# Kernel tuning notes

Measured on AMD Instinct MI355X. Metric: run time of the kernel, lower is better.

## Reference

```python
import jax, jax.numpy as jnp
import numpy as np

NUM_QUBITS = 16
N_LAYERS = 3
N_PARAMS = 6
BATCH = 64
DIM = 2 ** NUM_QUBITS


def setup_inputs() -> dict:
    key = jax.random.key(0)
    k1, k2, k3, k4, k5 = jax.random.split(key, 5)
    sr = jax.random.normal(k1, (BATCH, DIM), jnp.float32)
    si = jax.random.normal(k2, (BATCH, DIM), jnp.float32)
    nrm = jnp.sqrt(jnp.sum(sr * sr + si * si, axis=1, keepdims=True))
    sr, si = sr / nrm, si / nrm  # StatePrep requires normalized states
    var_params = jax.random.normal(k3, (N_LAYERS, NUM_QUBITS, N_PARAMS), jnp.float32)
    head_w = jax.random.normal(k4, (1, NUM_QUBITS), jnp.float32) / np.sqrt(NUM_QUBITS)
    head_b = jax.random.normal(k5, (1,), jnp.float32) * 0.01
    return {"state_real": sr, "state_imag": si, "var_params": var_params,
            "head_w": head_w, "head_b": head_b}


def _rot_unitary(tx, ty, tz):
    # Fused single-qubit unitary U = RZ(tz) @ RY(ty) @ RX(tx)
    cx, sx = jnp.cos(tx / 2), jnp.sin(tx / 2)
    cy, sy = jnp.cos(ty / 2), jnp.sin(ty / 2)
    Rx = jnp.stack([jnp.stack([cx + 0j, -1j * sx]),
                    jnp.stack([-1j * sx, cx + 0j])])
    Ry = jnp.stack([jnp.stack([cy + 0j, -sy + 0j]),
                    jnp.stack([sy + 0j, cy + 0j])])
    ez = jnp.exp(-1j * tz / 2)
    zero = jnp.zeros_like(ez)
    Rz = jnp.stack([jnp.stack([ez, zero]), jnp.stack([zero, jnp.conj(ez)])])
    return (Rz @ Ry @ Rx).astype(jnp.complex64)


def _circuit_features(state_real, state_imag, var_params):
    psi = jax.lax.complex(state_real, state_imag)  # (B, 2^n), wire 0 = MSB
    B = psi.shape[0]
    for l in range(N_LAYERS):
        for q in range(NUM_QUBITS):
            U = _rot_unitary(var_params[l, q, 0], var_params[l, q, 1], var_params[l, q, 2])
            psi = psi.reshape(B, 2 ** q, 2, -1)  # isolate wire q
            psi = jnp.einsum('ij,bljr->blir', U, psi)
        for q in range(NUM_QUBITS - 1):
            # CNOT(control=q, target=q+1): flip target axis where control=1
            psi = psi.reshape(B, 2 ** q, 2, 2, -1)
            psi = jnp.concatenate([psi[:, :, 0:1], psi[:, :, 1:2, ::-1]], axis=2)
        psi = psi.reshape(B, -1)
    probs = psi.real ** 2 + psi.imag ** 2  # (B, 2^n)
    feats = []
    for q in range(NUM_QUBITS):
        p = probs.reshape(B, 2 ** q, 2, -1)
        feats.append(p[:, :, 0, :].sum(axis=(1, 2)) - p[:, :, 1, :].sum(axis=(1, 2)))
    return jnp.stack(feats, axis=1)  # (B, n) expvals of PauliZ


def reference(state_real, state_imag, var_params, head_w, head_b):
    feats = _circuit_features(state_real, state_imag, var_params)
    return (feats @ head_w.T + head_b)[:, 0]  # (B,)
```

## Files before the change

kernel.cpp:

```cpp
#include <hip/hip_runtime.h>


typedef float f2 __attribute__((ext_vector_type(2)));

struct G8 { float r00,i00,r01,i01,r10,i10,r11,i11; };

__device__ __forceinline__ f2 mkf2(float a, float b) { f2 r; r.x = a; r.y = b; return r; }
__device__ __forceinline__ f2 swp(f2 v) { f2 r; r.x = v.y; r.y = v.x; return r; }
__device__ __forceinline__ f2 sn(f2 v) { f2 r; r.x = -v.y; r.y = v.x; return r; }
__device__ __forceinline__ f2 shf2(f2 v, int mask) {
  return mkf2(__shfl_xor(v.x, mask), __shfl_xor(v.y, mask));
}

__device__ __forceinline__ G8 loadG(const float* p) {
  G8 g;
  g.r00=p[0]; g.i00=p[1]; g.r01=p[2]; g.i01=p[3];
  g.r10=p[4]; g.i10=p[5]; g.r11=p[6]; g.i11=p[7];
  return g;
}

struct CP { f2 dr, di, br, bi; };
__device__ __forceinline__ CP mkCP(const G8& g, int w) {
  CP c;
  const float a = w ? g.r11 : g.r00, b = w ? g.i11 : g.i00;
  const float p = w ? g.r10 : g.r01, q = w ? g.i10 : g.i01;
  c.dr = mkf2(a,a); c.di = mkf2(b,b); c.br = mkf2(p,p); c.bi = mkf2(q,q);
  return c;
}
__device__ __forceinline__ void supdP(const CP& c, f2& x, f2 p) {
  x = __builtin_elementwise_fma(c.dr, x,
       __builtin_elementwise_fma(c.di, sn(x),
        __builtin_elementwise_fma(c.br, p, c.bi * sn(p))));
}

struct C2 { f2 dr, di, br, bi; };
__device__ __forceinline__ C2 mkC2(const G8& g, int wlo, int whi) {
  C2 c;
  c.dr = mkf2(wlo ? g.r11 : g.r00, whi ? g.r11 : g.r00);
  c.di = mkf2(wlo ? g.i11 : g.i00, whi ? g.i11 : g.i00);
  c.br = mkf2(wlo ? g.r10 : g.r01, whi ? g.r10 : g.r01);
  c.bi = mkf2(wlo ? g.i10 : g.i01, whi ? g.i10 : g.i01);
  return c;
}
__device__ __forceinline__ void supd2(const C2& c, f2& xr, f2& xi, f2 pr, f2 pi) {
  f2 nr = __builtin_elementwise_fma(c.dr, xr,
           __builtin_elementwise_fma(c.di, -xi,
            __builtin_elementwise_fma(c.br, pr, c.bi * (-pi))));
  f2 ni = __builtin_elementwise_fma(c.dr, xi,
           __builtin_elementwise_fma(c.di, xr,
            __builtin_elementwise_fma(c.br, pi, c.bi * pr)));
  xr = nr; xi = ni;
}

__device__ __forceinline__ void buildU(const float* __restrict__ vp, float* U) {
  const int i = threadIdx.x;
  if (i < 48) {
    const float tx = vp[i*6+0], ty = vp[i*6+1], tz = vp[i*6+2];
    float sx, cx, sy, cy, sz, cz;
    sincosf(0.5f*tx, &sx, &cx);
    sincosf(0.5f*ty, &sy, &cy);
    sincosf(0.5f*tz, &sz, &cz);
    const float m00r = cy*cx,  m00i = sy*sx;
    const float m01r = -sy*cx, m01i = -cy*sx;
    const float m10r = sy*cx,  m10i = -cy*sx;
    const float m11r = cy*cx,  m11i = -sy*sx;
    float* o = U + i*8;
    o[0] = cz*m00r + sz*m00i;  o[1] = cz*m00i - sz*m00r;
    o[2] = cz*m01r + sz*m01i;  o[3] = cz*m01i - sz*m01r;
    o[4] = cz*m10r - sz*m10i;  o[5] = cz*m10i + sz*m10r;
    o[6] = cz*m11r - sz*m11i;  o[7] = cz*m11i + sz*m11r;
  }
}

#define GU(l, w) loadG(Ush + ((l)*16 + (w))*8)

__global__ void __launch_bounds__(256, 2)
kA(const float* __restrict__ sr, const float* __restrict__ si,
   float* __restrict__ dr, float* __restrict__ di,
   const float* __restrict__ vp, const float* __restrict__ hb, float* __restrict__ out) {
  __shared__ float Ush[384];
  buildU(vp, Ush);
  const int t = threadIdx.x;
  const int l = t & 63, wv = t >> 6;
  const int l5 = (l >> 5) & 1, l4 = (l >> 4) & 1;
  const int b = blockIdx.x >> 3, c = blockIdx.x & 7;
  if (blockIdx.x == 0 && t < 64) out[t] = hb[0];
  __syncthreads();

  const size_t bb = (size_t)b << 16;
  const int tb = (l5 << 10) | (l4 << 9) | (c << 6) | (wv << 4) | (l & 15);
  f2 x[32];
  #pragma unroll
  for (int k = 0; k < 32; ++k) {
    const size_t a = bb + (k << 11) + tb;
    x[k] = mkf2(sr[a], si[a]);
  }

#define RPA(CA, CB, A, B) { f2 tt = x[A]; supdP(CA, x[A], x[B]); supdP(CB, x[B], tt); }

  #pragma unroll
  for (int g = 0; g < 5; ++g) {
    const int kb = 4 - g;
    const G8 U = GU(0, g);
    const CP c0 = mkCP(U, 0), c1 = mkCP(U, 1);
    #pragma unroll
    for (int p = 0; p < 16; ++p) {
      const int i0 = ((p >> kb) << (kb + 1)) | (p & ((1 << kb) - 1));
      RPA(c0, c1, i0, i0 | (1 << kb));
    }
  }
  { const G8 U = GU(0,5); const CP cc = mkCP(U, l5);
    #pragma unroll
    for (int a = 0; a < 32; ++a) supdP(cc, x[a], shf2(x[a], 32)); }
  { const G8 U = GU(0,6); const CP cc = mkCP(U, l4);
    #pragma unroll
    for (int a = 0; a < 32; ++a) supdP(cc, x[a], shf2(x[a], 16)); }
  { const G8 U = GU(1,0); const CP c0 = mkCP(U,0), c1 = mkCP(U,1);
    #pragma unroll
    for (int k = 0; k < 32; ++k) if (!((k>>4)&1)) RPA(c0, c1, k, k^24); }
  { const G8 U = GU(1,1); const CP c0 = mkCP(U,0), c1 = mkCP(U,1);
    #pragma unroll
    for (int k = 0; k < 32; ++k) if (!((k>>3)&1)) {
      const int f = (k>>4)&1;
      RPA(f?c1:c0, f?c0:c1, k, k^12);
    } }
  { const G8 U = GU(1,2); const CP c0 = mkCP(U,0), c1 = mkCP(U,1);
    #pragma unroll
    for (int k = 0; k < 32; ++k) if (!((k>>2)&1)) {
      const int f = ((k>>4)^(k>>3))&1;
      RPA(f?c1:c0, f?c0:c1, k, k^6);
    } }
  { const G8 U = GU(1,3); const CP c0 = mkCP(U,0), c1 = mkCP(U,1);
    #pragma unroll
    for (int k = 0; k < 32; ++k) if (!((k>>1)&1)) {
      const int f = ((k>>4)^(k>>3)^(k>>2))&1;
      RPA(f?c1:c0, f?c0:c1, k, k^3);
    } }
  { const G8 U = GU(1,4); const CP c0 = mkCP(U,0), c1 = mkCP(U,1);
    #pragma unroll
    for (int m = 0; m < 16; ++m) {
      const int k0 = 2*m, k1 = 2*m+1;
      f2 p0 = shf2(x[k1], 32), p1 = shf2(x[k0], 32);
      const int w0 = __builtin_popcount(k0)&1;
      supdP(w0?c1:c0, x[k0], p0);
      supdP(w0?c0:c1, x[k1], p1);
    } }
  { const G8 U = GU(2,0); const CP c0 = mkCP(U,0), c1 = mkCP(U,1);
    #pragma unroll
    for (int k = 0; k < 32; ++k) if (!((k>>4)&1)) RPA(c0, c1, k, k^20); }
  { const G8 U = GU(2,1); const CP c0 = mkCP(U,0), c1 = mkCP(U,1);
    #pragma unroll
    for (int k = 0; k < 32; ++k) if (!((k>>3)&1)) RPA(c0, c1, k, k^10); }
  { const G8 U = GU(2,2); const CP c0 = mkCP(U,0), c1 = mkCP(U,1);
    #pragma unroll
    for (int k = 0; k < 32; ++k) if (!((k>>2)&1)) {
      const int f = (k>>4)&1;
      RPA(f?c1:c0, f?c0:c1, k, k^5);
    } }

  #pragma unroll
  for (int k = 0; k < 32; ++k) {
    const size_t a = bb + (k << 11) + tb;
    dr[a] = x[k].x; di[a] = x[k].y;
  }
#undef RPA
}

__device__ __forceinline__ int SA2(int i) { return i ^ (((i >> 5) & 7) << 1); }

__global__ void __launch_bounds__(256, 2)
kB(const float* __restrict__ sr, const float* __restrict__ si,
   const float* __restrict__ vp, const float* __restrict__ hw, float* __restrict__ out) {
  __shared__ float lds[16384];
  __shared__ float Ush[384];
  __shared__ float red[4];
  buildU(vp, Ush);
  const int t = threadIdx.x;
  const int l = t & 63, wv = t >> 6;
  const int b = blockIdx.x >> 3, h3 = blockIdx.x & 7;
  __syncthreads();

  const int P   = __builtin_popcount(h3) & 1;
  const int h14 = (h3 >> 1) & 1;
  const int pA  = (h3 ^ (h3 >> 2)) & 1;
  const size_t base0 = ((size_t)b << 16) | (h3 << 13) | (wv << 8) | (l << 2);

  f2 xr2[16], xi2[16];
  #pragma unroll
  for (int kk = 0; kk < 4; ++kk) {
    const float4 r0 = *(const float4*)(sr + base0 + (kk << 10));
    const float4 r1 = *(const float4*)(sr + base0 + (kk << 10) + 4096);
    const float4 i0 = *(const float4*)(si + base0 + (kk << 10));
    const float4 i1 = *(const float4*)(si + base0 + (kk << 10) + 4096);
    xr2[kk*4+0] = mkf2(r0.x, r1.x); xr2[kk*4+1] = mkf2(r0.y, r1.y);
    xr2[kk*4+2] = mkf2(r0.z, r1.z); xr2[kk*4+3] = mkf2(r0.w, r1.w);
    xi2[kk*4+0] = mkf2(i0.x, i1.x); xi2[kk*4+1] = mkf2(i0.y, i1.y);
    xi2[kk*4+2] = mkf2(i0.z, i1.z); xi2[kk*4+3] = mkf2(i0.w, i1.w);
  }

#define RP2(CA, CB, A, B) { f2 tr = xr2[A], ti = xi2[A]; \
    supd2(CA, xr2[A], xi2[A], xr2[B], xi2[B]); \
    supd2(CB, xr2[B], xi2[B], tr, ti); }

  #pragma unroll
  for (int g = 0; g < 6; ++g) {
    const int mask = 32 >> g;
    const G8 U = GU(0, 8 + g);
    const int hi = (l >> (5 - g)) & 1;
    const C2 cc = mkC2(U, hi, hi);
    #pragma unroll
    for (int s = 0; s < 16; ++s) {
      f2 pr = shf2(xr2[s], mask), pi = shf2(xi2[s], mask);
      supd2(cc, xr2[s], xi2[s], pr, pi);
    }
  }
  { const G8 U = GU(0,14);
    const C2 c0 = mkC2(U,0,0), c1 = mkC2(U,1,1);
    #pragma unroll
    for (int kk = 0; kk < 4; ++kk)
      #pragma unroll
      for (int e0 = 0; e0 < 2; ++e0) RP2(c0, c1, kk*4+e0, kk*4+e0+2); }
  { const G8 U = GU(0,15);
    const C2 c0 = mkC2(U,0,0), c1 = mkC2(U,1,1);
    #pragma unroll
    for (int kk = 0; kk < 4; ++kk) {
      RP2(c0, c1, kk*4+0, kk*4+1);
      RP2(c0, c1, kk*4+2, kk*4+3);
    } }

  #pragma unroll
  for (int s = 0; s < 16; ++s) {
    const int i0 = (((s >> 2) << 10) | (wv << 8) | (l << 2) | (s & 3)) << 1;
    *(f2*)&lds[SA2(i0)] = xr2[s];
    *(f2*)&lds[8192 + SA2(i0)] = xi2[s];
  }
  __syncthreads();
  #pragma unroll
  for (int m = 0; m < 16; ++m) {
    const int i2 = (((m << 8) | (l << 2) | wv)) << 1;
    xr2[m] = *(f2*)&lds[SA2(i2)];
    xi2[m] = *(f2*)&lds[8192 + SA2(i2)];
  }

  const int l5=(l>>5)&1, l4=(l>>4)&1, l3=(l>>3)&1, l2=(l>>2)&1, l1=(l>>1)&1, l0=l&1;
  { const G8 U = GU(0,7);
    const C2 c0 = mkC2(U,0,0), c1 = mkC2(U,1,1);
    #pragma unroll
    for (int m = 0; m < 16; m += 2) RP2(c0, c1, m, m^1); }
  { const G8 U = GU(1,5);
    const C2 cA = mkC2(U, P, P^1), cB = mkC2(U, P^1, P);
    #pragma unroll
    for (int m = 0; m < 16; ++m) if (!((m>>2)&1)) {
      const int f = (m>>3)&1;
      RP2(f?cB:cA, f?cA:cB, m, m^6);
    } }
  { const G8 U = GU(1,6);
    const C2 cA = mkC2(U, P, P^1), cB = mkC2(U, P^1, P);
    #pragma unroll
    for (int m = 0; m < 16; ++m) if (!((m>>1)&1)) {
      const int f = ((m>>3)^(m>>2))&1;
      RP2(f?cB:cA, f?cA:cB, m, m^3);
    } }
  { const G8 U = GU(1,7);
    const C2 cA = mkC2(U, P, P^1), cB = mkC2(U, P^1, P);
    #pragma unroll
    for (int m = 0; m < 16; m += 2) {
      f2 p0r = shf2(xr2[m^1],32), p0i = shf2(xi2[m^1],32);
      f2 p1r = shf2(xr2[m],32),   p1i = shf2(xi2[m],32);
      const int f = __builtin_popcount(m)&1;
      supd2(f?cB:cA, xr2[m], xi2[m], p0r, p0i);
      supd2(f?cA:cB, xr2[m^1], xi2[m^1], p1r, p1i);
    } }
  #pragma unroll
  for (int g = 0; g < 5; ++g) {
    const int mask = 48 >> g;
    const G8 U = GU(1, 8 + g);
    const int lp = (g==0)? l5 : (g==1)? (l4^l5) : (g==2)? (l3^l4^l5)
                 : (g==3)? (l2^l3^l4^l5) : (l1^l2^l3^l4^l5);
    const C2 cA = mkC2(U, lp^P, lp^P^1), cB = mkC2(U, lp^P^1, lp^P);
    #pragma unroll
    for (int m = 0; m < 16; ++m) {
      f2 pr = shf2(xr2[m], mask), pi = shf2(xi2[m], mask);
      supd2((__builtin_popcount(m)&1)?cB:cA, xr2[m], xi2[m], pr, pi);
    }
  }
  { const G8 U = GU(2,3);
    const C2 cc = mkC2(U, h14, h14^1);
    #pragma unroll
    for (int m = 0; m < 16; ++m) if (!((m>>2)&1)) {
      f2 tr = xr2[m], ti = xi2[m];
      supd2(cc, xr2[m], xi2[m], swp(xr2[m^4]), swp(xi2[m^4]));
      supd2(cc, xr2[m^4], xi2[m^4], swp(tr), swp(ti));
    } }
  { const G8 U = GU(2,4);
    const C2 cA = mkC2(U, pA, pA), cB = mkC2(U, pA^1, pA^1);
    #pragma unroll
    for (int m = 0; m < 16; ++m) if (!((m>>3)&1)) RP2(cA, cB, m, m^10); }
  { const G8 U = GU(2,5);
    const C2 cA = mkC2(U, h14, h14^1), cB = mkC2(U, h14^1, h14);
    #pragma unroll
    for (int m = 0; m < 16; ++m) if (!((m>>2)&1)) RP2(cA, cB, m, m^5); }
  { const G8 U = GU(2,6);
    const C2 cA = mkC2(U, pA, pA), cB = mkC2(U, pA^1, pA^1);
    #pragma unroll
    for (int m = 0; m < 16; ++m) if (!((m>>1)&1)) {
      f2 p0r = shf2(xr2[m^2],32), p0i = shf2(xi2[m^2],32);
      f2 p1r = shf2(xr2[m],32),   p1i = shf2(xi2[m],32);
      const int f = (m>>3)&1;
      supd2(f?cB:cA, xr2[m], xi2[m], p0r, p0i);
      supd2(f?cA:cB, xr2[m^2], xi2[m^2], p1r, p1i);
    } }
  { const G8 U = GU(2,7);
    const C2 cA = mkC2(U, h14, h14^1), cB = mkC2(U, h14^1, h14);
    #pragma unroll
    for (int m = 0; m < 16; m += 2) {
      f2 p0r = shf2(xr2[m^1],16), p0i = shf2(xi2[m^1],16);
      f2 p1r = shf2(xr2[m],16),   p1i = shf2(xi2[m],16);
      const int f = (m>>2)&1;
      supd2(f?cB:cA, xr2[m], xi2[m], p0r, p0i);
      supd2(f?cA:cB, xr2[m^1], xi2[m^1], p1r, p1i);
    } }
  #pragma unroll
  for (int g = 0; g < 3; ++g) {
    const int mask = (g == 0) ? 40 : (g == 1) ? 20 : 10;
    const G8 U = GU(2, 8 + g);
    int lp, mpar, blo, bhi;
    if      (g == 0) { lp = l5;      mpar = 0x0A; blo = lp^pA;  bhi = lp^pA; }
    else if (g == 1) { lp = l4;      mpar = 0x05; blo = lp^h14; bhi = lp^h14^1; }
    else             { lp = l3^l5;   mpar = 0x0A; blo = lp^pA;  bhi = lp^pA; }
    const C2 cA = mkC2(U, blo, bhi), cB = mkC2(U, blo^1, bhi^1);
    #pragma unroll
    for (int m = 0; m < 16; ++m) {
      f2 pr = shf2(xr2[m], mask), pi = shf2(xi2[m], mask);
      supd2((__builtin_popcount(m & mpar)&1)?cB:cA, xr2[m], xi2[m], pr, pi);
    }
  }

  __syncthreads();
  #pragma unroll
  for (int m = 0; m < 16; ++m) {
    const int i2 = (((m << 8) | (l << 2) | wv)) << 1;
    *(f2*)&lds[SA2(i2)] = xr2[m];
    *(f2*)&lds[8192 + SA2(i2)] = xi2[m];
  }
  __syncthreads();
  #pragma unroll
  for (int s = 0; s < 16; ++s) {
    const int i0 = (((s >> 2) << 10) | (wv << 8) | (l << 2) | (s & 3)) << 1;
    xr2[s] = *(f2*)&lds[SA2(i0)];
    xi2[s] = *(f2*)&lds[8192 + SA2(i0)];
  }

  const int wv1 = (wv >> 1) & 1, wv0 = wv & 1;
  const int RPlo = (__builtin_popcount(l) ^ __builtin_popcount(wv) ^ P) & 1;
  const int oddT = (l1 ^ l3 ^ l5 ^ wv1 ^ pA) & 1;
  const int evlo = (l0 ^ l2 ^ l4 ^ wv0 ^ h14) & 1;
  { const G8 U = GU(1,13);
    const C2 cA = mkC2(U, RPlo, RPlo^1), cB = mkC2(U, RPlo^1, RPlo);
    #pragma unroll
    for (int kk = 0; kk < 4; ++kk) {
      const C2& cc = (__builtin_popcount(kk)&1) ? cB : cA;
      #pragma unroll
      for (int e0 = 0; e0 < 2; ++e0) {
        const int a = kk*4 + e0, a2 = a + 2;
        f2 par = shf2(xr2[a2],1), pai = shf2(xi2[a2],1);
        f2 pbr = shf2(xr2[a],1),  pbi = shf2(xi2[a],1);
        supd2(cc, xr2[a],  xi2[a],  par, pai);
        supd2(cc, xr2[a2], xi2[a2], pbr, pbi);
      }
    } }
  { const G8 U = GU(1,14);
    const C2 cA = mkC2(U, RPlo, RPlo^1), cB = mkC2(U, RPlo^1, RPlo);
    #pragma unroll
    for (int kk = 0; kk < 4; ++kk) {
      const int f = __builtin_popcount(kk)&1;
      RP2(f?cB:cA, f?cA:cB, kk*4+0, kk*4+3);
      RP2(f?cB:cA, f?cA:cB, kk*4+1, kk*4+2);
    } }
  { const G8 U = GU(1,15);
    const C2 cA = mkC2(U, RPlo, RPlo^1), cB = mkC2(U, RPlo^1, RPlo);
    #pragma unroll
    for (int kk = 0; kk < 4; ++kk) {
      const int f = __builtin_popcount(kk)&1;
      RP2(f?cB:cA, f?cA:cB, kk*4+0, kk*4+1);
      RP2(f?cA:cB, f?cB:cA, kk*4+2, kk*4+3);
    } }
  { const G8 U = GU(2,11);
    const int b4 = (l2 ^ l4 ^ wv0) & 1;
    const C2 cA = mkC2(U, b4^h14, b4^h14^1), cB = mkC2(U, b4^h14^1, b4^h14);
    #pragma unroll
    for (int s = 0; s < 16; ++s) {
      f2 pr = shf2(xr2[s], 5), pi = shf2(xi2[s], 5);
      supd2(((s>>2)&1)?cB:cA, xr2[s], xi2[s], pr, pi);
    } }
  { const G8 U = GU(2,12);
    const C2 cA = mkC2(U, oddT, oddT), cB = mkC2(U, oddT^1, oddT^1);
    #pragma unroll
    for (int kk = 0; kk < 4; ++kk) {
      const C2& cc = ((kk>>1)&1) ? cB : cA;
      #pragma unroll
      for (int e0 = 0; e0 < 2; ++e0) {
        const int a = kk*4 + e0, a2 = a + 2;
        f2 par = shf2(xr2[a2],2), pai = shf2(xi2[a2],2);
        f2 pbr = shf2(xr2[a],2),  pbi = shf2(xi2[a],2);
        supd2(cc, xr2[a],  xi2[a],  par, pai);
        supd2(cc, xr2[a2], xi2[a2], pbr, pbi);
      }
    } }
  { const G8 U = GU(2,13);
    const C2 cA = mkC2(U, evlo, evlo^1), cB = mkC2(U, evlo^1, evlo);
    #pragma unroll
    for (int kk = 0; kk < 4; ++kk) {
      const C2& cc = (kk&1) ? cB : cA;
      #pragma unroll
      for (int e0 = 0; e0 < 4; e0 += 2) {
        const int a = kk*4 + e0, a2 = a + 1;
        f2 par = shf2(xr2[a2],1), pai = shf2(xi2[a2],1);
        f2 pbr = shf2(xr2[a],1),  pbi = shf2(xi2[a],1);
        supd2(cc, xr2[a],  xi2[a],  par, pai);
        supd2(cc, xr2[a2], xi2[a2], pbr, pbi);
      }
    } }
  { const G8 U = GU(2,14);
    const C2 cA = mkC2(U, oddT, oddT), cB = mkC2(U, oddT^1, oddT^1);
    #pragma unroll
    for (int kk = 0; kk < 4; ++kk) {
      const int f = (kk>>1)&1;
      RP2(f?cB:cA, f?cA:cB, kk*4+0, kk*4+2);
      RP2(f?cB:cA, f?cA:cB, kk*4+1, kk*4+3);
    } }
  { const G8 U = GU(2,15);
    const C2 cA = mkC2(U, evlo, evlo^1), cB = mkC2(U, evlo^1, evlo);
    #pragma unroll
    for (int kk = 0; kk < 4; ++kk) {
      const int f = kk&1;
      RP2(f?cB:cA, f?cA:cB, kk*4+0, kk*4+1);
      RP2(f?cB:cA, f?cA:cB, kk*4+2, kk*4+3);
    } }

  #pragma unroll
  for (int s = 0; s < 16; ++s)
    xr2[s] = xr2[s]*xr2[s] + xi2[s]*xi2[s];
  const int jloc = (h3 << 13) | (wv << 8) | (l << 2);
  float hsum = 0.f;
  #pragma unroll
  for (int q = 0; q < 16; ++q) {
    const int M = (0x3333 << (15 - q)) & 0xFFFF;
    f2 acc = mkf2(0.f, 0.f);
    #pragma unroll
    for (int s = 0; s < 16; ++s) {
      const int amp = ((s >> 2) << 10) | (s & 3);
      if (__builtin_popcount(amp & M) & 1) acc -= xr2[s]; else acc += xr2[s];
    }
    float sv = acc.x + (((M >> 12) & 1) ? -acc.y : acc.y);
    if (__builtin_popcount(jloc & M) & 1) sv = -sv;
    hsum += hw[q] * sv;
  }
  #pragma unroll
  for (int o = 32; o >= 1; o >>= 1) hsum += __shfl_xor(hsum, o);
  if ((t & 63) == 0) red[wv] = hsum;
  __syncthreads();
  if (t == 0) atomicAdd(out + b, red[0] + red[1] + red[2] + red[3]);
#undef RP2
}

extern "C" void kernel_launch(void* const* d_in, const int* in_sizes, int n_in,
                              void* d_out, int out_size, void* d_ws, size_t ws_size,
                              hipStream_t stream) {
  const float* in_r = (const float*)d_in[0];
  const float* in_i = (const float*)d_in[1];
  const float* vp = (const float*)d_in[2];
  const float* hw = (const float*)d_in[3];
  const float* hb = (const float*)d_in[4];
  float* out = (float*)d_out;

  float* ws_r = (float*)d_ws;
  float* ws_i = ws_r + 4194304ull;

  kA<<<512, 256, 0, stream>>>(in_r, in_i, ws_r, ws_i, vp, hb, out);
  kB<<<512, 256, 0, stream>>>(ws_r, ws_i, vp, hw, out);
}
```

Measured before the change: 141.5 us.

## Split kB tiles in half and move two gates into kA

Moves gates (1,5) and (2,3) from the second kernel into the first, so one more wire becomes block-fixed in kB. kB can then give each block a 4096-amplitude slice instead of 8192, launching 1024 blocks with half the registers and LDS per thread and a launch bound of 4 blocks per CU. The intent is higher occupancy and better latency hiding in kB. The cost is more shuffle work in kA, and all the parity and index bookkeeping had to be re-derived, which risks correctness.

```diff
diff --git a/kernel.cpp b/kernel.cpp
--- a/kernel.cpp
+++ b/kernel.cpp
@@ -145,6 +145,12 @@
       supdP(w0?c1:c0, x[k0], p0);
       supdP(w0?c0:c1, x[k1], p1);
     } }
+  { const G8 U = GU(1,5); const CP cA = mkCP(U, l5), cB = mkCP(U, l5^1);
+    #pragma unroll
+    for (int k = 0; k < 32; ++k) {
+      f2 p = shf2(x[k], 48);
+      supdP((__builtin_popcount(k)&1)?cB:cA, x[k], p);
+    } }
   { const G8 U = GU(2,0); const CP c0 = mkCP(U,0), c1 = mkCP(U,1);
     #pragma unroll
     for (int k = 0; k < 32; ++k) if (!((k>>4)&1)) RPA(c0, c1, k, k^20); }
@@ -157,6 +163,14 @@
       const int f = (k>>4)&1;
       RPA(f?c1:c0, f?c0:c1, k, k^5);
     } }
+  { const G8 U = GU(2,3); const CP c0 = mkCP(U,0), c1 = mkCP(U,1);
+    #pragma unroll
+    for (int k = 0; k < 32; ++k) if (!((k>>1)&1)) {
+      f2 p0 = shf2(x[k^2], 32), p1 = shf2(x[k], 32);
+      const int f = (k>>3)&1;
+      supdP(f?c1:c0, x[k], p0);
+      supdP(f?c0:c1, x[k^2], p1);
+    } }
 
   #pragma unroll
   for (int k = 0; k < 32; ++k) {
@@ -168,30 +182,30 @@
 
 __device__ __forceinline__ int SA2(int i) { return i ^ (((i >> 5) & 7) << 1); }
 
-__global__ void __launch_bounds__(256, 2)
+__global__ void __launch_bounds__(256, 4)
 kB(const float* __restrict__ sr, const float* __restrict__ si,
    const float* __restrict__ vp, const float* __restrict__ hw, float* __restrict__ out) {
-  __shared__ float lds[16384];
+  __shared__ float lds[8192];
   __shared__ float Ush[384];
   __shared__ float red[4];
   buildU(vp, Ush);
   const int t = threadIdx.x;
   const int l = t & 63, wv = t >> 6;
-  const int b = blockIdx.x >> 3, h3 = blockIdx.x & 7;
-  __syncthreads();
-
-  const int P   = __builtin_popcount(h3) & 1;
-  const int h14 = (h3 >> 1) & 1;
-  const int pA  = (h3 ^ (h3 >> 2)) & 1;
-  const size_t base0 = ((size_t)b << 16) | (h3 << 13) | (wv << 8) | (l << 2);
-
-  f2 xr2[16], xi2[16];
-  #pragma unroll
-  for (int kk = 0; kk < 4; ++kk) {
+  const int b = blockIdx.x >> 4, h4 = blockIdx.x & 15;
+  __syncthreads();
+
+  const int ph4 = __builtin_popcount(h4) & 1;
+  const int pA4 = ((h4 >> 1) ^ (h4 >> 3)) & 1;
+  const int pB4 = (h4 ^ (h4 >> 2)) & 1;
+  const size_t base0 = ((size_t)b << 16) | (h4 << 12) | (wv << 8) | (l << 2);
+
+  f2 xr2[8], xi2[8];
+  #pragma unroll
+  for (int kk = 0; kk < 2; ++kk) {
     const float4 r0 = *(const float4*)(sr + base0 + (kk << 10));
-    const float4 r1 = *(const float4*)(sr + base0 + (kk << 10) + 4096);
+    const float4 r1 = *(const float4*)(sr + base0 + (kk << 10) + 2048);
     const float4 i0 = *(const float4*)(si + base0 + (kk << 10));
-    const float4 i1 = *(const float4*)(si + base0 + (kk << 10) + 4096);
+    const float4 i1 = *(const float4*)(si + base0 + (kk << 10) + 2048);
     xr2[kk*4+0] = mkf2(r0.x, r1.x); xr2[kk*4+1] = mkf2(r0.y, r1.y);
     xr2[kk*4+2] = mkf2(r0.z, r1.z); xr2[kk*4+3] = mkf2(r0.w, r1.w);
     xi2[kk*4+0] = mkf2(i0.x, i1.x); xi2[kk*4+1] = mkf2(i0.y, i1.y);
@@ -209,7 +223,7 @@
     const int hi = (l >> (5 - g)) & 1;
     const C2 cc = mkC2(U, hi, hi);
     #pragma unroll
-    for (int s = 0; s < 16; ++s) {
+    for (int s = 0; s < 8; ++s) {
       f2 pr = shf2(xr2[s], mask), pi = shf2(xi2[s], mask);
       supd2(cc, xr2[s], xi2[s], pr, pi);
     }
@@ -217,59 +231,54 @@
   { const G8 U = GU(0,14);
     const C2 c0 = mkC2(U,0,0), c1 = mkC2(U,1,1);
     #pragma unroll
-    for (int kk = 0; kk < 4; ++kk)
+    for (int kk = 0; kk < 2; ++kk)
       #pragma unroll
       for (int e0 = 0; e0 < 2; ++e0) RP2(c0, c1, kk*4+e0, kk*4+e0+2); }
   { const G8 U = GU(0,15);
     const C2 c0 = mkC2(U,0,0), c1 = mkC2(U,1,1);
     #pragma unroll
-    for (int kk = 0; kk < 4; ++kk) {
+    for (int kk = 0; kk < 2; ++kk) {
       RP2(c0, c1, kk*4+0, kk*4+1);
       RP2(c0, c1, kk*4+2, kk*4+3);
     } }
 
   #pragma unroll
-  for (int s = 0; s < 16; ++s) {
-    const int i0 = (((s >> 2) << 10) | (wv << 8) | (l << 2) | (s & 3)) << 1;
-    *(f2*)&lds[SA2(i0)] = xr2[s];
-    *(f2*)&lds[8192 + SA2(i0)] = xi2[s];
-  }
-  __syncthreads();
-  #pragma unroll
-  for (int m = 0; m < 16; ++m) {
-    const int i2 = (((m << 8) | (l << 2) | wv)) << 1;
-    xr2[m] = *(f2*)&lds[SA2(i2)];
-    xi2[m] = *(f2*)&lds[8192 + SA2(i2)];
+  for (int kk = 0; kk < 2; ++kk)
+    #pragma unroll
+    for (int e = 0; e < 4; ++e) {
+      const int fi = ((kk << 10) | (wv << 8) | (l << 2) | e) << 1;
+      *(f2*)&lds[SA2(fi)] = xr2[kk*4+e];
+      *(f2*)&lds[4096 + SA2(fi)] = xi2[kk*4+e];
+    }
+  __syncthreads();
+  #pragma unroll
+  for (int s3 = 0; s3 < 8; ++s3) {
+    const int fi = ((s3 << 8) | (l << 2) | wv) << 1;
+    xr2[s3] = *(f2*)&lds[SA2(fi)];
+    xi2[s3] = *(f2*)&lds[4096 + SA2(fi)];
   }
 
   const int l5=(l>>5)&1, l4=(l>>4)&1, l3=(l>>3)&1, l2=(l>>2)&1, l1=(l>>1)&1, l0=l&1;
   { const G8 U = GU(0,7);
     const C2 c0 = mkC2(U,0,0), c1 = mkC2(U,1,1);
     #pragma unroll
-    for (int m = 0; m < 16; m += 2) RP2(c0, c1, m, m^1); }
-  { const G8 U = GU(1,5);
-    const C2 cA = mkC2(U, P, P^1), cB = mkC2(U, P^1, P);
-    #pragma unroll
-    for (int m = 0; m < 16; ++m) if (!((m>>2)&1)) {
-      const int f = (m>>3)&1;
-      RP2(f?cB:cA, f?cA:cB, m, m^6);
-    } }
+    for (int s3 = 0; s3 < 8; s3 += 2) RP2(c0, c1, s3, s3^1); }
   { const G8 U = GU(1,6);
-    const C2 cA = mkC2(U, P, P^1), cB = mkC2(U, P^1, P);
-    #pragma unroll
-    for (int m = 0; m < 16; ++m) if (!((m>>1)&1)) {
-      const int f = ((m>>3)^(m>>2))&1;
-      RP2(f?cB:cA, f?cA:cB, m, m^3);
+    const C2 cA = mkC2(U, ph4, ph4^1), cB = mkC2(U, ph4^1, ph4);
+    #pragma unroll
+    for (int s3 = 0; s3 < 8; ++s3) if (!((s3>>1)&1)) {
+      const int f = (s3>>2)&1;
+      RP2(f?cB:cA, f?cA:cB, s3, s3^3);
     } }
   { const G8 U = GU(1,7);
-    const C2 cA = mkC2(U, P, P^1), cB = mkC2(U, P^1, P);
-    #pragma unroll
-    for (int m = 0; m < 16; m += 2) {
-      f2 p0r = shf2(xr2[m^1],32), p0i = shf2(xi2[m^1],32);
-      f2 p1r = shf2(xr2[m],32),   p1i = shf2(xi2[m],32);
-      const int f = __builtin_popcount(m)&1;
-      supd2(f?cB:cA, xr2[m], xi2[m], p0r, p0i);
-      supd2(f?cA:cB, xr2[m^1], xi2[m^1], p1r, p1i);
+    const C2 cA = mkC2(U, ph4, ph4^1), cB = mkC2(U, ph4^1, ph4);
+    #pragma unroll
+    for (int s3 = 0; s3 < 8; s3 += 2) {
+      f2 p0r = shf2(xr2[s3^1],32), p0i = shf2(xi2[s3^1],32);
+      f2 p1r = shf2(xr2[s3],32),   p1i = shf2(xi2[s3],32);
+      const int f = ((s3>>2)^(s3>>1))&1;
+      supd2(f?cB:cA, xr2[s3], xi2[s3], p0r, p0i);
+      supd2(f?cA:cB, xr2[s3^1], xi2[s3^1], p1r, p1i);
     } }
   #pragma unroll
   for (int g = 0; g < 5; ++g) {
@@ -277,89 +286,87 @@
     const G8 U = GU(1, 8 + g);
     const int lp = (g==0)? l5 : (g==1)? (l4^l5) : (g==2)? (l3^l4^l5)
                  : (g==3)? (l2^l3^l4^l5) : (l1^l2^l3^l4^l5);
-    const C2 cA = mkC2(U, lp^P, lp^P^1), cB = mkC2(U, lp^P^1, lp^P);
-    #pragma unroll
-    for (int m = 0; m < 16; ++m) {
-      f2 pr = shf2(xr2[m], mask), pi = shf2(xi2[m], mask);
-      supd2((__builtin_popcount(m)&1)?cB:cA, xr2[m], xi2[m], pr, pi);
-    }
-  }
-  { const G8 U = GU(2,3);
-    const C2 cc = mkC2(U, h14, h14^1);
-    #pragma unroll
-    for (int m = 0; m < 16; ++m) if (!((m>>2)&1)) {
-      f2 tr = xr2[m], ti = xi2[m];
-      supd2(cc, xr2[m], xi2[m], swp(xr2[m^4]), swp(xi2[m^4]));
-      supd2(cc, xr2[m^4], xi2[m^4], swp(tr), swp(ti));
-    } }
+    const C2 cA = mkC2(U, (lp^ph4)&1, (lp^ph4^1)&1);
+    const C2 cB = mkC2(U, (lp^ph4^1)&1, (lp^ph4)&1);
+    #pragma unroll
+    for (int s3 = 0; s3 < 8; ++s3) {
+      f2 pr = shf2(xr2[s3], mask), pi = shf2(xi2[s3], mask);
+      supd2((__builtin_popcount(s3)&1)?cB:cA, xr2[s3], xi2[s3], pr, pi);
+    }
+  }
   { const G8 U = GU(2,4);
-    const C2 cA = mkC2(U, pA, pA), cB = mkC2(U, pA^1, pA^1);
-    #pragma unroll
-    for (int m = 0; m < 16; ++m) if (!((m>>3)&1)) RP2(cA, cB, m, m^10); }
+    const C2 cc = mkC2(U, pA4, pA4^1);
+    #pragma unroll
+    for (int s3 = 0; s3 < 8; ++s3) if (!((s3>>1)&1)) {
+      f2 tr = xr2[s3], ti = xi2[s3];
+      supd2(cc, xr2[s3], xi2[s3], swp(xr2[s3^2]), swp(xi2[s3^2]));
+      supd2(cc, xr2[s3^2], xi2[s3^2], swp(tr), swp(ti));
+    } }
   { const G8 U = GU(2,5);
-    const C2 cA = mkC2(U, h14, h14^1), cB = mkC2(U, h14^1, h14);
-    #pragma unroll
-    for (int m = 0; m < 16; ++m) if (!((m>>2)&1)) RP2(cA, cB, m, m^5); }
+    const C2 cA = mkC2(U, pB4, pB4), cB = mkC2(U, pB4^1, pB4^1);
+    #pragma unroll
+    for (int s3 = 0; s3 < 4; ++s3) RP2(cA, cB, s3, s3^5); }
   { const G8 U = GU(2,6);
-    const C2 cA = mkC2(U, pA, pA), cB = mkC2(U, pA^1, pA^1);
-    #pragma unroll
-    for (int m = 0; m < 16; ++m) if (!((m>>1)&1)) {
-      f2 p0r = shf2(xr2[m^2],32), p0i = shf2(xi2[m^2],32);
-      f2 p1r = shf2(xr2[m],32),   p1i = shf2(xi2[m],32);
-      const int f = (m>>3)&1;
-      supd2(f?cB:cA, xr2[m], xi2[m], p0r, p0i);
-      supd2(f?cA:cB, xr2[m^2], xi2[m^2], p1r, p1i);
+    const C2 cA = mkC2(U, pA4, pA4^1), cB = mkC2(U, pA4^1, pA4);
+    #pragma unroll
+    for (int s3 = 0; s3 < 8; ++s3) if (!((s3>>1)&1)) {
+      f2 p0r = shf2(xr2[s3^2],32), p0i = shf2(xi2[s3^2],32);
+      f2 p1r = shf2(xr2[s3],32),   p1i = shf2(xi2[s3],32);
+      supd2(cA, xr2[s3], xi2[s3], p0r, p0i);
+      supd2(cB, xr2[s3^2], xi2[s3^2], p1r, p1i);
     } }
   { const G8 U = GU(2,7);
-    const C2 cA = mkC2(U, h14, h14^1), cB = mkC2(U, h14^1, h14);
-    #pragma unroll
-    for (int m = 0; m < 16; m += 2) {
-      f2 p0r = shf2(xr2[m^1],16), p0i = shf2(xi2[m^1],16);
-      f2 p1r = shf2(xr2[m],16),   p1i = shf2(xi2[m],16);
-      const int f = (m>>2)&1;
-      supd2(f?cB:cA, xr2[m], xi2[m], p0r, p0i);
-      supd2(f?cA:cB, xr2[m^1], xi2[m^1], p1r, p1i);
+    const C2 cA = mkC2(U, pB4, pB4), cB = mkC2(U, pB4^1, pB4^1);
+    #pragma unroll
+    for (int s3 = 0; s3 < 8; s3 += 2) {
+      f2 p0r = shf2(xr2[s3^1],16), p0i = shf2(xi2[s3^1],16);
+      f2 p1r = shf2(xr2[s3],16),   p1i = shf2(xi2[s3],16);
+      const int f = (s3>>2)&1;
+      supd2(f?cB:cA, xr2[s3], xi2[s3], p0r, p0i);
+      supd2(f?cA:cB, xr2[s3^1], xi2[s3^1], p1r, p1i);
     } }
   #pragma unroll
   for (int g = 0; g < 3; ++g) {
     const int mask = (g == 0) ? 40 : (g == 1) ? 20 : 10;
     const G8 U = GU(2, 8 + g);
-    int lp, mpar, blo, bhi;
-    if      (g == 0) { lp = l5;      mpar = 0x0A; blo = lp^pA;  bhi = lp^pA; }
-    else if (g == 1) { lp = l4;      mpar = 0x05; blo = lp^h14; bhi = lp^h14^1; }
-    else             { lp = l3^l5;   mpar = 0x0A; blo = lp^pA;  bhi = lp^pA; }
+    int mpar, blo, bhi;
+    if      (g == 0) { mpar = 2; blo = (l5^pA4)&1;      bhi = blo^1; }
+    else if (g == 1) { mpar = 5; blo = (l4^pB4)&1;      bhi = blo;   }
+    else             { mpar = 2; blo = (l3^l5^pA4)&1;   bhi = blo^1; }
     const C2 cA = mkC2(U, blo, bhi), cB = mkC2(U, blo^1, bhi^1);
     #pragma unroll
-    for (int m = 0; m < 16; ++m) {
-      f2 pr = shf2(xr2[m], mask), pi = shf2(xi2[m], mask);
-      supd2((__builtin_popcount(m & mpar)&1)?cB:cA, xr2[m], xi2[m], pr, pi);
-    }
-  }
-
-  __syncthreads();
-  #pragma unroll
-  for (int m = 0; m < 16; ++m) {
-    const int i2 = (((m << 8) | (l << 2) | wv)) << 1;
-    *(f2*)&lds[SA2(i2)] = xr2[m];
-    *(f2*)&lds[8192 + SA2(i2)] = xi2[m];
-  }
-  __syncthreads();
-  #pragma unroll
-  for (int s = 0; s < 16; ++s) {
-    const int i0 = (((s >> 2) << 10) | (wv << 8) | (l << 2) | (s & 3)) << 1;
-    xr2[s] = *(f2*)&lds[SA2(i0)];
-    xi2[s] = *(f2*)&lds[8192 + SA2(i0)];
-  }
+    for (int s3 = 0; s3 < 8; ++s3) {
+      f2 pr = shf2(xr2[s3], mask), pi = shf2(xi2[s3], mask);
+      supd2((__builtin_popcount(s3 & mpar)&1)?cB:cA, xr2[s3], xi2[s3], pr, pi);
+    }
+  }
+
+  __syncthreads();
+  #pragma unroll
+  for (int s3 = 0; s3 < 8; ++s3) {
+    const int fi = ((s3 << 8) | (l << 2) | wv) << 1;
+    *(f2*)&lds[SA2(fi)] = xr2[s3];
+    *(f2*)&lds[4096 + SA2(fi)] = xi2[s3];
+  }
+  __syncthreads();
+  #pragma unroll
+  for (int kk = 0; kk < 2; ++kk)
+    #pragma unroll
+    for (int e = 0; e < 4; ++e) {
+      const int fi = ((kk << 10) | (wv << 8) | (l << 2) | e) << 1;
+      xr2[kk*4+e] = *(f2*)&lds[SA2(fi)];
+      xi2[kk*4+e] = *(f2*)&lds[4096 + SA2(fi)];
+    }
 
   const int wv1 = (wv >> 1) & 1, wv0 = wv & 1;
-  const int RPlo = (__builtin_popcount(l) ^ __builtin_popcount(wv) ^ P) & 1;
-  const int oddT = (l1 ^ l3 ^ l5 ^ wv1 ^ pA) & 1;
-  const int evlo = (l0 ^ l2 ^ l4 ^ wv0 ^ h14) & 1;
+  const int RPlo  = (__builtin_popcount(l) ^ __builtin_popcount(wv) ^ ph4) & 1;
+  const int oddTl = (l1 ^ l3 ^ l5 ^ wv1 ^ pA4) & 1;
+  const int evB   = (l0 ^ l2 ^ l4 ^ wv0 ^ pB4) & 1;
   { const G8 U = GU(1,13);
     const C2 cA = mkC2(U, RPlo, RPlo^1), cB = mkC2(U, RPlo^1, RPlo);
     #pragma unroll
-    for (int kk = 0; kk < 4; ++kk) {
-      const C2& cc = (__builtin_popcount(kk)&1) ? cB : cA;
+    for (int kk = 0; kk < 2; ++kk) {
+      const C2& cc = kk ? cB : cA;
       #pragma unroll
       for (int e0 = 0; e0 < 2; ++e0) {
         const int a = kk*4 + e0, a2 = a + 2;
@@ -372,32 +379,29 @@
   { const G8 U = GU(1,14);
     const C2 cA = mkC2(U, RPlo, RPlo^1), cB = mkC2(U, RPlo^1, RPlo);
     #pragma unroll
-    for (int kk = 0; kk < 4; ++kk) {
-      const int f = __builtin_popcount(kk)&1;
-      RP2(f?cB:cA, f?cA:cB, kk*4+0, kk*4+3);
-      RP2(f?cB:cA, f?cA:cB, kk*4+1, kk*4+2);
+    for (int kk = 0; kk < 2; ++kk) {
+      RP2(kk?cB:cA, kk?cA:cB, kk*4+0, kk*4+3);
+      RP2(kk?cB:cA, kk?cA:cB, kk*4+1, kk*4+2);
     } }
   { const G8 U = GU(1,15);
     const C2 cA = mkC2(U, RPlo, RPlo^1), cB = mkC2(U, RPlo^1, RPlo);
     #pragma unroll
-    for (int kk = 0; kk < 4; ++kk) {
-      const int f = __builtin_popcount(kk)&1;
-      RP2(f?cB:cA, f?cA:cB, kk*4+0, kk*4+1);
-      RP2(f?cA:cB, f?cB:cA, kk*4+2, kk*4+3);
+    for (int kk = 0; kk < 2; ++kk) {
+      RP2(kk?cB:cA, kk?cA:cB, kk*4+0, kk*4+1);
+      RP2(kk?cA:cB, kk?cB:cA, kk*4+2, kk*4+3);
     } }
   { const G8 U = GU(2,11);
-    const int b4 = (l2 ^ l4 ^ wv0) & 1;
-    const C2 cA = mkC2(U, b4^h14, b4^h14^1), cB = mkC2(U, b4^h14^1, b4^h14);
-    #pragma unroll
-    for (int s = 0; s < 16; ++s) {
+    const int b4 = (l2 ^ l4 ^ wv0 ^ pB4) & 1;
+    const C2 cA = mkC2(U, b4, b4), cB = mkC2(U, b4^1, b4^1);
+    #pragma unroll
+    for (int s = 0; s < 8; ++s) {
       f2 pr = shf2(xr2[s], 5), pi = shf2(xi2[s], 5);
-      supd2(((s>>2)&1)?cB:cA, xr2[s], xi2[s], pr, pi);
+      supd2((s>>2)?cB:cA, xr2[s], xi2[s], pr, pi);
     } }
   { const G8 U = GU(2,12);
-    const C2 cA = mkC2(U, oddT, oddT), cB = mkC2(U, oddT^1, oddT^1);
-    #pragma unroll
-    for (int kk = 0; kk < 4; ++kk) {
-      const C2& cc = ((kk>>1)&1) ? cB : cA;
+    const C2 cc = mkC2(U, oddTl, oddTl^1);
+    #pragma unroll
+    for (int kk = 0; kk < 2; ++kk)
       #pragma unroll
       for (int e0 = 0; e0 < 2; ++e0) {
         const int a = kk*4 + e0, a2 = a + 2;
@@ -405,13 +409,12 @@
         f2 pbr = shf2(xr2[a],2),  pbi = shf2(xi2[a],2);
         supd2(cc, xr2[a],  xi2[a],  par, pai);
         supd2(cc, xr2[a2], xi2[a2], pbr, pbi);
-      }
-    } }
+      } }
   { const G8 U = GU(2,13);
-    const C2 cA = mkC2(U, evlo, evlo^1), cB = mkC2(U, evlo^1, evlo);
-    #pragma unroll
-    for (int kk = 0; kk < 4; ++kk) {
-      const C2& cc = (kk&1) ? cB : cA;
+    const C2 cA = mkC2(U, evB, evB), cB = mkC2(U, evB^1, evB^1);
+    #pragma unroll
+    for (int kk = 0; kk < 2; ++kk) {
+      const C2& cc = kk ? cB : cA;
       #pragma unroll
       for (int e0 = 0; e0 < 4; e0 += 2) {
         const int a = kk*4 + e0, a2 = a + 1;
@@ -422,37 +425,35 @@
       }
     } }
   { const G8 U = GU(2,14);
-    const C2 cA = mkC2(U, oddT, oddT), cB = mkC2(U, oddT^1, oddT^1);
-    #pragma unroll
-    for (int kk = 0; kk < 4; ++kk) {
-      const int f = (kk>>1)&1;
-      RP2(f?cB:cA, f?cA:cB, kk*4+0, kk*4+2);
-      RP2(f?cB:cA, f?cA:cB, kk*4+1, kk*4+3);
+    const C2 cA = mkC2(U, oddTl, oddTl^1), cB = mkC2(U, oddTl^1, oddTl);
+    #pragma unroll
+    for (int kk = 0; kk < 2; ++kk) {
+      RP2(cA, cB, kk*4+0, kk*4+2);
+      RP2(cA, cB, kk*4+1, kk*4+3);
     } }
   { const G8 U = GU(2,15);
-    const C2 cA = mkC2(U, evlo, evlo^1), cB = mkC2(U, evlo^1, evlo);
-    #pragma unroll
-    for (int kk = 0; kk < 4; ++kk) {
-      const int f = kk&1;
-      RP2(f?cB:cA, f?cA:cB, kk*4+0, kk*4+1);
-      RP2(f?cB:cA, f?cA:cB, kk*4+2, kk*4+3);
-    } }
-
-  #pragma unroll
-  for (int s = 0; s < 16; ++s)
+    const C2 cA = mkC2(U, evB, evB), cB = mkC2(U, evB^1, evB^1);
+    #pragma unroll
+    for (int kk = 0; kk < 2; ++kk) {
+      RP2(kk?cB:cA, kk?cA:cB, kk*4+0, kk*4+1);
+      RP2(kk?cB:cA, kk?cA:cB, kk*4+2, kk*4+3);
+    } }
+
+  #pragma unroll
+  for (int s = 0; s < 8; ++s)
     xr2[s] = xr2[s]*xr2[s] + xi2[s]*xi2[s];
-  const int jloc = (h3 << 13) | (wv << 8) | (l << 2);
+  const int jloc = (h4 << 12) | (wv << 8) | (l << 2);
   float hsum = 0.f;
   #pragma unroll
   for (int q = 0; q < 16; ++q) {
     const int M = (0x3333 << (15 - q)) & 0xFFFF;
     f2 acc = mkf2(0.f, 0.f);
     #pragma unroll
-    for (int s = 0; s < 16; ++s) {
+    for (int s = 0; s < 8; ++s) {
       const int amp = ((s >> 2) << 10) | (s & 3);
       if (__builtin_popcount(amp & M) & 1) acc -= xr2[s]; else acc += xr2[s];
     }
-    float sv = acc.x + (((M >> 12) & 1) ? -acc.y : acc.y);
+    float sv = acc.x + (((M >> 11) & 1) ? -acc.y : acc.y);
     if (__builtin_popcount(jloc & M) & 1) sv = -sv;
     hsum += hw[q] * sv;
   }
@@ -477,6 +478,6 @@
   float* ws_r = (float*)d_ws;
   float* ws_i = ws_r + 4194304ull;
 
-  kA<<<512, 256, 0, stream>>>(in_r, in_i, ws_r, ws_i, vp, hb, out);
-  kB<<<512, 256, 0, stream>>>(ws_r, ws_i, vp, hw, out);
-}
+  kA<<<512,  256, 0, stream>>>(in_r, in_i, ws_r, ws_i, vp, hb, out);
+  kB<<<1024, 256, 0, stream>>>(ws_r, ws_i, vp, hw, out);
+}
```

Result: no change. 142.7 us (+0.9%).
